# Kernel optimization log

Measured on AMD Instinct MI355X. Metric: run time of the kernel, lower is better.

## Reference

```python
import jax, jax.numpy as jnp
import numpy as np

B, S, K_IN = 8, 2048, 512
D_MODEL = 1024
N_INPUT = 2048
N_PROCESS = 4096
HIDDEN = 4096  # default hidden_dim = n_input * 2
K = 256


def setup_inputs() -> dict:
    key = jax.random.key(0)
    ks = jax.random.split(key, 7)
    return {
        "selected_activations": jax.random.normal(ks[0], (B, S, K_IN), dtype=jnp.float32),
        "selected_indices": jax.random.randint(ks[1], (B, K_IN), 0, N_INPUT),
        "k": K,
        "combination_weights": jax.random.normal(ks[2], (N_PROCESS, N_INPUT), dtype=jnp.float32) * np.float32(np.sqrt(2.0 / N_INPUT)),
        "output_projections": jax.random.normal(ks[3], (N_PROCESS, D_MODEL), dtype=jnp.float32) * np.float32(np.sqrt(2.0 / N_PROCESS)),
        "w1": jax.random.normal(ks[4], (HIDDEN, N_INPUT), dtype=jnp.float32) * np.float32(np.sqrt(2.0 / (N_INPUT + HIDDEN))),
        "b1": jnp.zeros((HIDDEN,), dtype=jnp.float32),
        "w2": jax.random.normal(ks[5], (N_PROCESS, HIDDEN), dtype=jnp.float32) * np.float32(np.sqrt(2.0 / (HIDDEN + N_PROCESS))),
        "b2": jnp.zeros((N_PROCESS,), dtype=jnp.float32),
    }


def reference(selected_activations, selected_indices, k, combination_weights,
              output_projections, w1, b1, w2, b2):
    bsz = selected_indices.shape[0]
    n_input = combination_weights.shape[1]

    # Per-batch gather of combination weights: [B, k_in, n_process]
    sel_w = combination_weights.T[selected_indices]

    # Process activations: [B, S, n_process], exact (erf) GELU like torch F.gelu
    process_activations = jax.nn.gelu(
        jnp.einsum('bsk,bkp->bsp', selected_activations, sel_w), approximate=False)

    # One-hot style input-selection mask via scatter: [B, n_input]
    input_selection = jnp.zeros((bsz, n_input), dtype=jnp.float32)
    input_selection = input_selection.at[jnp.arange(bsz)[:, None], selected_indices].set(1.0)

    # Combination analyzer MLP: Linear -> GELU -> Linear
    h = jax.nn.gelu(input_selection @ w1.T + b1, approximate=False)
    combination_relevance = h @ w2.T + b2  # [B, n_process]

    # Router scores and top-k process selection
    activation_scores = process_activations.max(axis=1)  # [B, n_process]
    final_scores = activation_scores * jax.nn.sigmoid(combination_relevance)
    _, process_indices = jax.lax.top_k(final_scores, k)  # [B, k]

    # Gather selected process activations [B, S, k] and projections [B, k, d_model]
    sel_pa = jnp.take_along_axis(process_activations, process_indices[:, None, :], axis=2)
    sel_proj = output_projections[process_indices]

    # Final projection: [B, S, d_model]
    return jnp.einsum('bsk,bkd->bsd', sel_pa, sel_proj)
```

## Files before the change

kernel.cpp:

```cpp
#include <hip/hip_runtime.h>
#include <math.h>

#define B 8
#define S 2048
#define KIN 512
#define NIN 2048
#define NP 4096
#define HID 4096
#define DM 1024
#define TOPK 256

typedef __bf16 bf16x8 __attribute__((ext_vector_type(8)));
typedef __bf16 bf16x4 __attribute__((ext_vector_type(4)));
typedef float f32x4 __attribute__((ext_vector_type(4)));

__device__ __forceinline__ float gelu_exact(float x) {
    return 0.5f * x * (1.0f + erff(x * 0.70710678118654752440f));
}

__device__ __forceinline__ void atomicMaxFloat(float* addr, float val) {
    if (val >= 0.0f) atomicMax((int*)addr, __float_as_int(val));
    else             atomicMin((unsigned int*)addr, __float_as_uint(val));
}

__device__ __forceinline__ void async_copy16(void* lds, const void* g) {
    __builtin_amdgcn_global_load_lds(
        (__attribute__((address_space(1))) void*)g,
        (__attribute__((address_space(3))) void*)lds, 16, 0, 0);
}

__global__ __launch_bounds__(256) void init_kernel(float* scores, float* relacc,
                                                   float* hacc, unsigned* maskb,
                                                   int* selcnt) {
    int t = blockIdx.x * blockDim.x + threadIdx.x;
    if (t < B * NP)  { scores[t] = __int_as_float(0xFF800000); relacc[t] = 0.f; }
    if (t < B * HID) hacc[t] = 0.f;
    if (t < NIN)     maskb[t] = 0u;
    if (t < B)       selcnt[t] = 0;
}

__global__ __launch_bounds__(256) void scatter_maskbits(const int* __restrict__ idx,
                                                        unsigned* __restrict__ maskb) {
    int t = blockIdx.x * blockDim.x + threadIdx.x;
    if (t >= B * KIN) return;
    int b = t / KIN;
    atomicOr(&maskb[idx[t]], 1u << b);
}

__global__ __launch_bounds__(256) void pack_A(const float* __restrict__ A,
                                              __bf16* __restrict__ Apack) {
    size_t t = (size_t)blockIdx.x * 256 + threadIdx.x;
    size_t f = t * 4;
    size_t rowi = f >> 9;
    int j = (int)(f & 511);
    float4 v = *(const float4*)(A + f);
    __bf16 h0 = (__bf16)v.x, h1 = (__bf16)v.y, h2 = (__bf16)v.z, h3 = (__bf16)v.w;
    bf16x4 hv = {h0, h1, h2, h3};
    bf16x4 lv = {(__bf16)(v.x - (float)h0), (__bf16)(v.y - (float)h1),
                 (__bf16)(v.z - (float)h2), (__bf16)(v.w - (float)h3)};
    __bf16* orow = Apack + rowi * 1024;
    *(bf16x4*)(orow + j) = hv;
    *(bf16x4*)(orow + 512 + j) = lv;
}

__global__ __launch_bounds__(256) void gather_pack_w(const float* __restrict__ cw,
                                                     const int* __restrict__ idx,
                                                     __bf16* __restrict__ wpack) {
    __shared__ float rowbuf[4][NIN];
    __shared__ int sidx[B][KIN];
    int p0 = blockIdx.x * 4;
    int tid = threadIdx.x;
    for (int t = tid; t < B * KIN; t += 256) sidx[t >> 9][t & 511] = idx[t];
#pragma unroll
    for (int r = 0; r < 4; ++r)
        for (int c = tid; c < NIN / 4; c += 256)
            *(float4*)&rowbuf[r][c * 4] = *(const float4*)&cw[(size_t)(p0 + r) * NIN + c * 4];
    __syncthreads();
#pragma unroll
    for (int r = 0; r < 4; ++r) {
        int p = p0 + r;
        for (int b = 0; b < B; ++b) {
            __bf16* orow = wpack + ((size_t)b * NP + p) * 1024;
            for (int j = tid; j < KIN; j += 256) {
                float x = rowbuf[r][sidx[b][j]];
                __bf16 hh = (__bf16)x;
                orow[j] = hh;
                orow[512 + j] = (__bf16)(x - (float)hh);
            }
        }
    }
}

template <int EPI, int NSEG, int KSEG, int LDA, int LDB, int BROWS, int LDOUT>
__global__ __launch_bounds__(256) void mfma_gemm(const __bf16* __restrict__ Ap,
                                                 const __bf16* __restrict__ Bp,
                                                 void* __restrict__ outp) {
    __shared__ __align__(16) __bf16 As[128 * 64];
    __shared__ __align__(16) __bf16 Ws[128 * 64];
    const int b = blockIdx.z;
    const int s0 = blockIdx.x * 128;
    const int p0 = blockIdx.y * 128;
    const int tid = threadIdx.x;
    const int w = tid >> 6, lane = tid & 63;
    const int wr = w >> 1, wc = w & 1;
    const int ldRow = lane >> 3;
    const int ldCol = ((lane & 7) ^ (ldRow & 7)) * 8;
    const int fr = lane & 15;
    const int fq = lane >> 4;
    const __bf16* Ab = Ap + ((size_t)b * S + s0) * LDA;
    const __bf16* Bb = Bp + ((size_t)b * BROWS + p0) * LDB;

    f32x4 acc[4][4] = {};

    for (int seg = 0; seg < NSEG; ++seg) {
        const int aoff = (seg == 1) ? KSEG : 0;
        const int boff = (seg == 2) ? KSEG : 0;
        for (int k0 = 0; k0 < KSEG; k0 += 64) {
            __syncthreads();
#pragma unroll
            for (int i = 0; i < 4; ++i) {
                const __bf16* g = Ab + (size_t)(w * 32 + i * 8 + ldRow) * LDA + aoff + k0 + ldCol;
                async_copy16(&As[(w * 32 + i * 8) * 64], g);
            }
#pragma unroll
            for (int i = 0; i < 4; ++i) {
                const __bf16* g = Bb + (size_t)(w * 32 + i * 8 + ldRow) * LDB + boff + k0 + ldCol;
                async_copy16(&Ws[(w * 32 + i * 8) * 64], g);
            }
            __syncthreads();
#pragma unroll
            for (int ks = 0; ks < 2; ++ks) {
                bf16x8 af[4], bfr[4];
#pragma unroll
                for (int i = 0; i < 4; ++i) {
                    int R = wr * 64 + i * 16 + fr;
                    af[i] = *(const bf16x8*)&As[R * 64 + (((ks * 4 + fq) ^ (R & 7)) * 8)];
                }
#pragma unroll
                for (int j = 0; j < 4; ++j) {
                    int R = wc * 64 + j * 16 + fr;
                    bfr[j] = *(const bf16x8*)&Ws[R * 64 + (((ks * 4 + fq) ^ (R & 7)) * 8)];
                }
#pragma unroll
                for (int i = 0; i < 4; ++i)
#pragma unroll
                    for (int j = 0; j < 4; ++j)
                        acc[i][j] = __builtin_amdgcn_mfma_f32_16x16x32_bf16(af[i], bfr[j], acc[i][j], 0, 0, 0);
            }
        }
    }

    if constexpr (EPI == 1) {
        __bf16* o = (__bf16*)outp;
#pragma unroll
        for (int i = 0; i < 4; ++i)
#pragma unroll
            for (int r = 0; r < 4; ++r) {
                size_t row = (size_t)b * S + s0 + wr * 64 + i * 16 + fq * 4 + r;
#pragma unroll
                for (int j = 0; j < 4; ++j)
                    o[row * LDOUT + p0 + wc * 64 + j * 16 + fr] = (__bf16)gelu_exact(acc[i][j][r]);
            }
    } else {
        float* o = (float*)outp;
#pragma unroll
        for (int i = 0; i < 4; ++i)
#pragma unroll
            for (int r = 0; r < 4; ++r) {
                size_t row = (size_t)b * S + s0 + wr * 64 + i * 16 + fq * 4 + r;
#pragma unroll
                for (int j = 0; j < 4; ++j)
                    o[row * LDOUT + p0 + wc * 64 + j * 16 + fr] = acc[i][j][r];
            }
    }
}

__device__ __forceinline__ void stage64(__bf16* ldsTile, const __bf16* gRow0,
                                        int rbase, int ldg, int koff, int w, int lane) {
    const int rr = lane >> 3;
    const int gc = ((lane & 7) ^ rr) * 8;
    const __bf16* g = gRow0 + (size_t)(rbase + w * 8 + rr) * ldg + (koff + gc);
    async_copy16(ldsTile + (rbase + w * 8) * 64, g);
}

template <int EPI, int NSEG, int KSEG, int LDA, int LDB, int BROWS, int LDOUT>
__global__ __launch_bounds__(512, 2) void mfma_gemm256(const __bf16* __restrict__ Ap,
                                                       const __bf16* __restrict__ Bp,
                                                       void* __restrict__ outp) {
    constexpr int TPS = KSEG / 64;
    constexpr int NT = NSEG * TPS;
    __shared__ __align__(16) __bf16 As[2][256 * 64];
    __shared__ __align__(16) __bf16 Ws[2][256 * 64];

    const int flat = blockIdx.x + (blockIdx.y << 3) + (blockIdx.z << 7);
    const int b = flat & 7;
    const int j = flat >> 3;
    const int s0 = (j & 7) * 256;
    const int p0 = (j >> 3) * 256;

    const int tid = threadIdx.x;
    const int w = tid >> 6, lane = tid & 63;
    const int wr = w >> 2, wc = w & 3;
    const int fr = lane & 15, fq = lane >> 4;
    const __bf16* Ab = Ap + ((size_t)b * S + s0) * LDA;
    const __bf16* Bb = Bp + ((size_t)b * BROWS + p0) * LDB;

    auto offs = [&](int t, int& ao, int& bo) {
        int seg = t / TPS, k0 = (t % TPS) * 64;
        ao = ((NSEG == 3 && seg == 1) ? KSEG : 0) + k0;
        bo = ((NSEG == 3 && seg == 2) ? KSEG : 0) + k0;
    };

    int offA[2][2][4];
    int offB[2][4];
#pragma unroll
    for (int kk = 0; kk < 2; ++kk) {
#pragma unroll
        for (int mh = 0; mh < 2; ++mh)
#pragma unroll
            for (int mi = 0; mi < 4; ++mi) {
                int R = wr * 128 + mh * 64 + mi * 16 + fr;
                offA[kk][mh][mi] = R * 64 + (((kk * 4 + fq) ^ (R & 7)) * 8);
            }
#pragma unroll
        for (int nj = 0; nj < 4; ++nj) {
            int R = wc * 64 + nj * 16 + fr;
            offB[kk][nj] = R * 64 + (((kk * 4 + fq) ^ (R & 7)) * 8);
        }
    }

    f32x4 acc[8][4] = {};

    {
        int ao, bo;
        offs(0, ao, bo);
        stage64(&As[0][0], Ab, 0, LDA, ao, w, lane);
        stage64(&As[0][0], Ab, 128, LDA, ao, w, lane);
        stage64(&As[0][0], Ab, 64, LDA, ao, w, lane);
        stage64(&As[0][0], Ab, 192, LDA, ao, w, lane);
        stage64(&Ws[0][0], Bb, 0, LDB, bo, w, lane);
        stage64(&Ws[0][0], Bb, 128, LDB, bo, w, lane);
        stage64(&Ws[0][0], Bb, 64, LDB, bo, w, lane);
        stage64(&Ws[0][0], Bb, 192, LDB, bo, w, lane);
        if (NT > 1) {
            offs(1, ao, bo);
            stage64(&As[1][0], Ab, 0, LDA, ao, w, lane);
            stage64(&As[1][0], Ab, 128, LDA, ao, w, lane);
            stage64(&Ws[1][0], Bb, 0, LDB, bo, w, lane);
            stage64(&Ws[1][0], Bb, 128, LDB, bo, w, lane);
            asm volatile("s_waitcnt vmcnt(4)" ::: "memory");
        } else {
            asm volatile("s_waitcnt vmcnt(0)" ::: "memory");
        }
        __builtin_amdgcn_s_barrier();
    }

    for (int t = 0; t < NT; ++t) {
        const __bf16* Asb = &As[t & 1][0];
        const __bf16* Wsb = &Ws[t & 1][0];
        __bf16* Asn = &As[(t & 1) ^ 1][0];
        __bf16* Wsn = &Ws[(t & 1) ^ 1][0];
        bf16x8 af[4], bfr[4];

        af[0] = *(const bf16x8*)&Asb[offA[0][0][0]];
#pragma unroll
        for (int n = 0; n < 4; ++n) bfr[n] = *(const bf16x8*)&Wsb[offB[0][n]];
#pragma unroll
        for (int i = 1; i < 4; ++i) af[i] = *(const bf16x8*)&Asb[offA[0][0][i]];
        if (t + 1 < NT) {
            int ao, bo;
            offs(t + 1, ao, bo);
            stage64(Asn, Ab, 64, LDA, ao, w, lane);
            stage64(Asn, Ab, 192, LDA, ao, w, lane);
            stage64(Wsn, Bb, 64, LDB, bo, w, lane);
            stage64(Wsn, Bb, 192, LDB, bo, w, lane);
        }
        __builtin_amdgcn_s_barrier();
        __builtin_amdgcn_s_setprio(1);
#pragma unroll
        for (int mi = 0; mi < 4; ++mi)
#pragma unroll
            for (int nj = 0; nj < 4; ++nj)
                acc[mi][nj] = __builtin_amdgcn_mfma_f32_16x16x32_bf16(af[mi], bfr[nj], acc[mi][nj], 0, 0, 0);
        __builtin_amdgcn_s_setprio(0);
        __builtin_amdgcn_s_barrier();

#pragma unroll
        for (int i = 0; i < 4; ++i) af[i] = *(const bf16x8*)&Asb[offA[0][1][i]];
        __builtin_amdgcn_s_barrier();
        __builtin_amdgcn_s_setprio(1);
#pragma unroll
        for (int mi = 0; mi < 4; ++mi)
#pragma unroll
            for (int nj = 0; nj < 4; ++nj)
                acc[4 + mi][nj] = __builtin_amdgcn_mfma_f32_16x16x32_bf16(af[mi], bfr[nj], acc[4 + mi][nj], 0, 0, 0);
        __builtin_amdgcn_s_setprio(0);
        __builtin_amdgcn_s_barrier();

        af[0] = *(const bf16x8*)&Asb[offA[1][0][0]];
#pragma unroll
        for (int n = 0; n < 4; ++n) bfr[n] = *(const bf16x8*)&Wsb[offB[1][n]];
#pragma unroll
        for (int i = 1; i < 4; ++i) af[i] = *(const bf16x8*)&Asb[offA[1][0][i]];
        __builtin_amdgcn_s_barrier();
        __builtin_amdgcn_s_setprio(1);
#pragma unroll
        for (int mi = 0; mi < 4; ++mi)
#pragma unroll
            for (int nj = 0; nj < 4; ++nj)
                acc[mi][nj] = __builtin_amdgcn_mfma_f32_16x16x32_bf16(af[mi], bfr[nj], acc[mi][nj], 0, 0, 0);
        __builtin_amdgcn_s_setprio(0);
        __builtin_amdgcn_s_barrier();

#pragma unroll
        for (int i = 0; i < 4; ++i) af[i] = *(const bf16x8*)&Asb[offA[1][1][i]];
        if (t + 2 < NT) {
            int ao, bo;
            offs(t + 2, ao, bo);
            stage64((__bf16*)Asb, Ab, 0, LDA, ao, w, lane);
            stage64((__bf16*)Asb, Ab, 128, LDA, ao, w, lane);
            stage64((__bf16*)Wsb, Bb, 0, LDB, bo, w, lane);
            stage64((__bf16*)Wsb, Bb, 128, LDB, bo, w, lane);
            asm volatile("s_waitcnt vmcnt(4)" ::: "memory");
        } else {
            asm volatile("s_waitcnt vmcnt(0)" ::: "memory");
        }
        __builtin_amdgcn_s_barrier();
        __builtin_amdgcn_s_setprio(1);
#pragma unroll
        for (int mi = 0; mi < 4; ++mi)
#pragma unroll
            for (int nj = 0; nj < 4; ++nj)
                acc[4 + mi][nj] = __builtin_amdgcn_mfma_f32_16x16x32_bf16(af[mi], bfr[nj], acc[4 + mi][nj], 0, 0, 0);
        __builtin_amdgcn_s_setprio(0);
        __builtin_amdgcn_s_barrier();
    }

    if constexpr (EPI == 0) {
        float* scores = (float*)outp;
#pragma unroll
        for (int nj = 0; nj < 4; ++nj) {
            float mx = -INFINITY, mn = INFINITY;
#pragma unroll
            for (int mi = 0; mi < 8; ++mi)
#pragma unroll
                for (int r = 0; r < 4; ++r) {
                    float v = acc[mi][nj][r];
                    mx = fmaxf(mx, v);
                    mn = fminf(mn, v);
                }
            mx = fmaxf(mx, __shfl_xor(mx, 16));
            mx = fmaxf(mx, __shfl_xor(mx, 32));
            mn = fminf(mn, __shfl_xor(mn, 16));
            mn = fminf(mn, __shfl_xor(mn, 32));
            if (fq == 0) {
                float m = fmaxf(gelu_exact(mx), gelu_exact(mn));
                atomicMaxFloat(&scores[(size_t)b * LDOUT + p0 + wc * 64 + nj * 16 + fr], m);
            }
        }
    } else if constexpr (EPI == 1) {
        __bf16* o = (__bf16*)outp;
#pragma unroll
        for (int mi = 0; mi < 8; ++mi)
#pragma unroll
            for (int r = 0; r < 4; ++r) {
                size_t row = (size_t)b * S + s0 + wr * 128 + mi * 16 + fq * 4 + r;
#pragma unroll
                for (int nj = 0; nj < 4; ++nj)
                    o[row * LDOUT + p0 + wc * 64 + nj * 16 + fr] = (__bf16)gelu_exact(acc[mi][nj][r]);
            }
    } else {
        float* o = (float*)outp;
#pragma unroll
        for (int mi = 0; mi < 8; ++mi)
#pragma unroll
            for (int r = 0; r < 4; ++r) {
                size_t row = (size_t)b * S + s0 + wr * 128 + mi * 16 + fq * 4 + r;
#pragma unroll
                for (int nj = 0; nj < 4; ++nj)
                    o[row * LDOUT + p0 + wc * 64 + nj * 16 + fr] = acc[mi][nj][r];
            }
    }
}

__global__ __launch_bounds__(256) void mlp1_part(const float* __restrict__ w1,
                                                 const unsigned* __restrict__ maskb,
                                                 float* __restrict__ hacc) {
    __shared__ unsigned smb[512];
    int i0 = blockIdx.x * 64;
    int c0 = blockIdx.y * 512;
    int tid = threadIdx.x;
    for (int c = tid; c < 512; c += 256) smb[c] = maskb[c0 + c];
    __syncthreads();
    int r = tid >> 2, cq = tid & 3;
    const float* row = w1 + (size_t)(i0 + r) * NIN + c0;
    float acc[B] = {};
    for (int it = 0; it < 32; ++it) {
        int c = it * 16 + cq * 4;
        float4 v = *(const float4*)(row + c);
        float vv[4] = {v.x, v.y, v.z, v.w};
#pragma unroll
        for (int e = 0; e < 4; ++e) {
            unsigned mb = smb[c + e];
#pragma unroll
            for (int bb = 0; bb < B; ++bb)
                if (mb & (1u << bb)) acc[bb] += vv[e];
        }
    }
#pragma unroll
    for (int bb = 0; bb < B; ++bb)
        atomicAdd(&hacc[bb * HID + i0 + r], acc[bb]);
}

__global__ __launch_bounds__(256) void fin1(const float* __restrict__ hacc,
                                            const float* __restrict__ b1,
                                            float* __restrict__ h) {
    int t = blockIdx.x * 256 + threadIdx.x;
    if (t < B * HID) h[t] = gelu_exact(hacc[t] + b1[t & (HID - 1)]);
}

__global__ __launch_bounds__(256) void mlp2_part(const float* __restrict__ w2,
                                                 const float* __restrict__ h,
                                                 float* __restrict__ relacc) {
    __shared__ float sh[B][512];
    int p0 = blockIdx.x * 64;
    int c0 = blockIdx.y * 512;
    int tid = threadIdx.x;
    for (int i = tid; i < B * 128; i += 256) {
        int bb = i >> 7, c4 = i & 127;
        *(float4*)&sh[bb][c4 * 4] = *(const float4*)&h[(size_t)bb * HID + c0 + c4 * 4];
    }
    __syncthreads();
    int r = tid >> 2, cq = tid & 3;
    const float* row = w2 + (size_t)(p0 + r) * HID + c0;
    float acc[B] = {};
    for (int it = 0; it < 32; ++it) {
        int c = it * 16 + cq * 4;
        float4 v = *(const float4*)(row + c);
#pragma unroll
        for (int bb = 0; bb < B; ++bb)
            acc[bb] += v.x * sh[bb][c] + v.y * sh[bb][c + 1] + v.z * sh[bb][c + 2] + v.w * sh[bb][c + 3];
    }
#pragma unroll
    for (int bb = 0; bb < B; ++bb)
        atomicAdd(&relacc[bb * NP + p0 + r], acc[bb]);
}

__global__ __launch_bounds__(256) void topk_select(const float* __restrict__ scores,
                                                   const float* __restrict__ relacc,
                                                   const float* __restrict__ b2,
                                                   int* __restrict__ selidx,
                                                   int* __restrict__ selcnt) {
    __shared__ float sc[NP];
    int b = blockIdx.y;
    int p = blockIdx.x * 256 + threadIdx.x;
    for (int c = threadIdx.x; c < NP; c += 256) {
        float rel = relacc[(size_t)b * NP + c] + b2[c];
        sc[c] = scores[(size_t)b * NP + c] * (1.0f / (1.0f + expf(-rel)));
    }
    __syncthreads();
    float my = sc[p];
    int cnt = 0;
    for (int q = 0; q < NP; ++q) {
        float v = sc[q];
        cnt += (v > my) || (v == my && q < p);
    }
    if (cnt < TOPK) {
        int pos = atomicAdd(&selcnt[b], 1);
        selidx[b * TOPK + pos] = p;
    }
}

__global__ __launch_bounds__(256) void wsel_gather(const __bf16* __restrict__ wpack,
                                                   const int* __restrict__ selidx,
                                                   __bf16* __restrict__ wsel) {
    int kk = blockIdx.x, b = blockIdx.y;
    int sel = selidx[b * TOPK + kk];
    const unsigned* src = (const unsigned*)(wpack + ((size_t)b * NP + sel) * 1024);
    unsigned* dst = (unsigned*)(wsel + ((size_t)b * TOPK + kk) * 512);
    dst[threadIdx.x] = src[threadIdx.x];
}

__global__ __launch_bounds__(256) void projT_gather(const float* __restrict__ proj,
                                                    const int* __restrict__ selidx,
                                                    __bf16* __restrict__ PT) {
    __shared__ float tile[64][68];
    __shared__ int sel[64];
    int b = blockIdx.z, d0 = blockIdx.x * 64, k0 = blockIdx.y * 64;
    int tid = threadIdx.x;
    if (tid < 64) sel[tid] = selidx[b * TOPK + k0 + tid];
    __syncthreads();
    for (int r = 0; r < 4; ++r) {
        int kk = r * 16 + (tid >> 4);
        float4 v = *(const float4*)&proj[(size_t)sel[kk] * DM + d0 + (tid & 15) * 4];
        *(float4*)&tile[kk][(tid & 15) * 4] = v;
    }
    __syncthreads();
    for (int r = 0; r < 16; ++r) {
        int dd = r * 4 + (tid >> 6);
        int kk = tid & 63;
        PT[((size_t)b * DM + d0 + dd) * TOPK + k0 + kk] = (__bf16)tile[kk][dd];
    }
}

extern "C" void kernel_launch(void* const* d_in, const int* in_sizes, int n_in,
                              void* d_out, int out_size, void* d_ws, size_t ws_size,
                              hipStream_t stream) {
    const float* A    = (const float*)d_in[0];
    const int*   idx  = (const int*)d_in[1];
    const float* cw   = (const float*)d_in[3];
    const float* proj = (const float*)d_in[4];
    const float* w1   = (const float*)d_in[5];
    const float* b1   = (const float*)d_in[6];
    const float* w2   = (const float*)d_in[7];
    const float* b2   = (const float*)d_in[8];
    float* out = (float*)d_out;

    char* ws = (char*)d_ws;
    size_t off = 0;
    auto alloc = [&](size_t bytes) {
        void* p = ws + off;
        off += (bytes + 255) & ~(size_t)255;
        return p;
    };
    __bf16* Apack = (__bf16*)alloc((size_t)B * S * 1024 * 2);
    __bf16* Wpack = (__bf16*)alloc((size_t)B * NP * 1024 * 2);
    __bf16* selpa = (__bf16*)alloc((size_t)B * S * TOPK * 2);
    __bf16* PT    = (__bf16*)alloc((size_t)B * DM * TOPK * 2);
    __bf16* Wsel  = (__bf16*)alloc((size_t)B * TOPK * 512 * 2);
    float* scores = (float*)alloc((size_t)B * NP * 4);
    float* relacc = (float*)alloc((size_t)B * NP * 4);
    float* hacc   = (float*)alloc((size_t)B * HID * 4);
    float* h      = (float*)alloc((size_t)B * HID * 4);
    unsigned* maskb = (unsigned*)alloc((size_t)NIN * 4);
    int* selidx   = (int*)alloc((size_t)B * TOPK * 4);
    int* selcnt   = (int*)alloc((size_t)B * 4);

    init_kernel<<<dim3((B * HID + 255) / 256), 256, 0, stream>>>(scores, relacc, hacc, maskb, selcnt);
    scatter_maskbits<<<dim3((B * KIN + 255) / 256), 256, 0, stream>>>(idx, maskb);
    pack_A<<<dim3((B * S * KIN / 4) / 256), 256, 0, stream>>>(A, Apack);
    gather_pack_w<<<dim3(NP / 4), 256, 0, stream>>>(cw, idx, Wpack);

    mfma_gemm256<0, 3, 512, 1024, 1024, NP, NP>
        <<<dim3(S / 256, NP / 256, B), 512, 0, stream>>>(Apack, Wpack, (void*)scores);

    mlp1_part<<<dim3(HID / 64, NIN / 512), 256, 0, stream>>>(w1, maskb, hacc);
    fin1<<<dim3((B * HID + 255) / 256), 256, 0, stream>>>(hacc, b1, h);
    mlp2_part<<<dim3(NP / 64, HID / 512), 256, 0, stream>>>(w2, h, relacc);

    topk_select<<<dim3(NP / 256, B), 256, 0, stream>>>(scores, relacc, b2, selidx, selcnt);

    wsel_gather<<<dim3(TOPK, B), 256, 0, stream>>>(Wpack, selidx, Wsel);
    projT_gather<<<dim3(DM / 64, TOPK / 64, B), 256, 0, stream>>>(proj, selidx, PT);

    mfma_gemm<1, 1, 512, 1024, 512, TOPK, TOPK>
        <<<dim3(S / 128, TOPK / 128, B), 256, 0, stream>>>(Apack, Wsel, (void*)selpa);

    mfma_gemm<2, 1, 256, 256, 256, DM, DM>
        <<<dim3(S / 128, DM / 128, B), 256, 0, stream>>>(selpa, PT, (void*)out);
}
```

Before: 655.5 us.

## Vectorize weight pack stores, fuse GELU into mlp2, vectorize top-k counting

The weight gather-pack kernel now has each thread build 8 bf16 hi/lo values and write them with 16-byte vector stores, replacing scalar 2-byte stores. The separate fin1 kernel is removed: mlp2_part applies bias plus exact GELU while loading the hidden activations into shared memory, saving a launch and a round trip through global memory, though each block now recomputes GELU for its slice. The top-k rank counting loop reads shared memory as float4 and uses four independent counters to raise ILP.

```diff
diff --git a/kernel.cpp b/kernel.cpp
--- a/kernel.cpp
+++ b/kernel.cpp
@@ -77,17 +77,21 @@
             *(float4*)&rowbuf[r][c * 4] = *(const float4*)&cw[(size_t)(p0 + r) * NIN + c * 4];
     __syncthreads();
 #pragma unroll
-    for (int r = 0; r < 4; ++r) {
-        int p = p0 + r;
-        for (int b = 0; b < B; ++b) {
-            __bf16* orow = wpack + ((size_t)b * NP + p) * 1024;
-            for (int j = tid; j < KIN; j += 256) {
-                float x = rowbuf[r][sidx[b][j]];
-                __bf16 hh = (__bf16)x;
-                orow[j] = hh;
-                orow[512 + j] = (__bf16)(x - (float)hh);
-            }
-        }
+    for (int it = 0; it < 8; ++it) {
+        int combo = it * 4 + (tid >> 6);
+        int r = combo >> 3, bb = combo & 7;
+        int j0 = (tid & 63) * 8;
+        bf16x8 hv, lv;
+#pragma unroll
+        for (int e = 0; e < 8; ++e) {
+            float x = rowbuf[r][sidx[bb][j0 + e]];
+            __bf16 hh = (__bf16)x;
+            hv[e] = hh;
+            lv[e] = (__bf16)(x - (float)hh);
+        }
+        __bf16* orow = wpack + ((size_t)bb * NP + p0 + r) * 1024;
+        *(bf16x8*)(orow + j0) = hv;
+        *(bf16x8*)(orow + 512 + j0) = lv;
     }
 }
 
@@ -412,15 +416,9 @@
         atomicAdd(&hacc[bb * HID + i0 + r], acc[bb]);
 }
 
-__global__ __launch_bounds__(256) void fin1(const float* __restrict__ hacc,
-                                            const float* __restrict__ b1,
-                                            float* __restrict__ h) {
-    int t = blockIdx.x * 256 + threadIdx.x;
-    if (t < B * HID) h[t] = gelu_exact(hacc[t] + b1[t & (HID - 1)]);
-}
-
 __global__ __launch_bounds__(256) void mlp2_part(const float* __restrict__ w2,
-                                                 const float* __restrict__ h,
+                                                 const float* __restrict__ hacc,
+                                                 const float* __restrict__ b1,
                                                  float* __restrict__ relacc) {
     __shared__ float sh[B][512];
     int p0 = blockIdx.x * 64;
@@ -428,7 +426,12 @@
     int tid = threadIdx.x;
     for (int i = tid; i < B * 128; i += 256) {
         int bb = i >> 7, c4 = i & 127;
-        *(float4*)&sh[bb][c4 * 4] = *(const float4*)&h[(size_t)bb * HID + c0 + c4 * 4];
+        float4 a = *(const float4*)&hacc[(size_t)bb * HID + c0 + c4 * 4];
+        float4 bias = *(const float4*)&b1[c0 + c4 * 4];
+        sh[bb][c4 * 4 + 0] = gelu_exact(a.x + bias.x);
+        sh[bb][c4 * 4 + 1] = gelu_exact(a.y + bias.y);
+        sh[bb][c4 * 4 + 2] = gelu_exact(a.z + bias.z);
+        sh[bb][c4 * 4 + 3] = gelu_exact(a.w + bias.w);
     }
     __syncthreads();
     int r = tid >> 2, cq = tid & 3;
@@ -451,7 +454,7 @@
                                                    const float* __restrict__ b2,
                                                    int* __restrict__ selidx,
                                                    int* __restrict__ selcnt) {
-    __shared__ float sc[NP];
+    __shared__ __align__(16) float sc[NP];
     int b = blockIdx.y;
     int p = blockIdx.x * 256 + threadIdx.x;
     for (int c = threadIdx.x; c < NP; c += 256) {
@@ -460,11 +463,18 @@
     }
     __syncthreads();
     float my = sc[p];
-    int cnt = 0;
-    for (int q = 0; q < NP; ++q) {
-        float v = sc[q];
-        cnt += (v > my) || (v == my && q < p);
-    }
+    int cnt0 = 0, cnt1 = 0, cnt2 = 0, cnt3 = 0;
+    const float4* s4 = (const float4*)sc;
+#pragma unroll 8
+    for (int i = 0; i < NP / 4; ++i) {
+        float4 v = s4[i];
+        int q = i * 4;
+        cnt0 += (int)(v.x > my) | ((int)(v.x == my) & (int)(q < p));
+        cnt1 += (int)(v.y > my) | ((int)(v.y == my) & (int)(q + 1 < p));
+        cnt2 += (int)(v.z > my) | ((int)(v.z == my) & (int)(q + 2 < p));
+        cnt3 += (int)(v.w > my) | ((int)(v.w == my) & (int)(q + 3 < p));
+    }
+    int cnt = (cnt0 + cnt1) + (cnt2 + cnt3);
     if (cnt < TOPK) {
         int pos = atomicAdd(&selcnt[b], 1);
         selidx[b * TOPK + pos] = p;
@@ -531,7 +541,6 @@
     float* scores = (float*)alloc((size_t)B * NP * 4);
     float* relacc = (float*)alloc((size_t)B * NP * 4);
     float* hacc   = (float*)alloc((size_t)B * HID * 4);
-    float* h      = (float*)alloc((size_t)B * HID * 4);
     unsigned* maskb = (unsigned*)alloc((size_t)NIN * 4);
     int* selidx   = (int*)alloc((size_t)B * TOPK * 4);
     int* selcnt   = (int*)alloc((size_t)B * 4);
@@ -545,8 +554,7 @@
         <<<dim3(S / 256, NP / 256, B), 512, 0, stream>>>(Apack, Wpack, (void*)scores);
 
     mlp1_part<<<dim3(HID / 64, NIN / 512), 256, 0, stream>>>(w1, maskb, hacc);
-    fin1<<<dim3((B * HID + 255) / 256), 256, 0, stream>>>(hacc, b1, h);
-    mlp2_part<<<dim3(NP / 64, HID / 512), 256, 0, stream>>>(w2, h, relacc);
+    mlp2_part<<<dim3(NP / 64, HID / 512), 256, 0, stream>>>(w2, hacc, b1, relacc);
 
     topk_select<<<dim3(NP / 256, B), 256, 0, stream>>>(scores, relacc, b2, selidx, selcnt);
 
```

After: 634.1 us. 3.3% less time.
